# Performance work log

Hardware: AMD Instinct MI355X
Metric: run time of the kernel (lower is better)

The kernel has to match this reference:

```python
import jax, jax.numpy as jnp
import numpy as np

EPS = 1e-6
SCALING = 32 ** -0.5  # key_dim ** -0.5


def _ln(x, g, b):
    m = jnp.mean(x, -1, keepdims=True)
    v = jnp.var(x, -1, keepdims=True)
    return (x - m) * jax.lax.rsqrt(v + EPS) * g + b


def _dwconv(x, w, b, pad):
    # x: (B,H,W,C); w: (kh,kw,1,C) depthwise kernel
    y = jax.lax.conv_general_dilated(
        x, w, (1, 1), [(pad, pad), (pad, pad)],
        dimension_numbers=("NHWC", "HWIO", "NHWC"),
        feature_group_count=x.shape[-1])
    return y + b


def _rotate_every_two(x):
    x1 = x[..., ::2]
    x2 = x[..., 1::2]
    return jnp.stack([-x2, x1], axis=-1).reshape(x.shape)


def _theta_shift(x, sin, cos):
    return x * cos + _rotate_every_two(x) * sin


def setup_inputs() -> dict:
    key = jax.random.key(0)
    ks = jax.random.split(key, 32)
    B, H, W, C = 2, 56, 56, 256
    N, D = 8, C // 8          # heads, key_dim
    F = 1024                  # ffn_dim
    L = H * W
    g = 2 ** -2.5
    inp = {
        "x": jax.random.normal(ks[0], (B, H, W, C), jnp.float32),
        "sin": jax.random.normal(ks[1], (H, W, D), jnp.float32),
        "cos": jax.random.normal(ks[2], (H, W, D), jnp.float32),
        "mask": jax.random.normal(ks[3], (N, L, L), jnp.float32),
        # pos dwconv 3x3
        "pos_w": jax.random.normal(ks[4], (3, 3, 1, C), jnp.float32) * 0.05,
        "pos_b": jnp.zeros((C,), jnp.float32),
        # retention layernorm
        "ln1_g": jnp.ones((C,), jnp.float32),
        "ln1_b": jnp.zeros((C,), jnp.float32),
        # q/k/v projections (stored as (in,out))
        "wq": jax.random.normal(ks[5], (C, C), jnp.float32) * g * (2.0 / (C + C)) ** 0.5 * 10,
        "bq": jnp.zeros((C,), jnp.float32),
        "wk": jax.random.normal(ks[6], (C, C), jnp.float32) * g * 0.06,
        "bk": jnp.zeros((C,), jnp.float32),
        "wv": jax.random.normal(ks[7], (C, C), jnp.float32) * g * 0.06,
        "bv": jnp.zeros((C,), jnp.float32),
        # lepe dwconv 5x5
        "lepe_w": jax.random.normal(ks[8], (5, 5, 1, C), jnp.float32) * 0.05,
        "lepe_b": jnp.zeros((C,), jnp.float32),
        # out proj
        "wo": jax.random.normal(ks[9], (C, C), jnp.float32) * 0.06,
        "bo": jnp.zeros((C,), jnp.float32),
        # final layernorm
        "ln2_g": jnp.ones((C,), jnp.float32),
        "ln2_b": jnp.zeros((C,), jnp.float32),
        # ffn
        "w1": jax.random.normal(ks[10], (C, F), jnp.float32) * 0.04,
        "b1": jnp.zeros((F,), jnp.float32),
        "ffn_w": jax.random.normal(ks[11], (3, 3, 1, F), jnp.float32) * 0.05,
        "ffn_b": jnp.zeros((F,), jnp.float32),
        "w2": jax.random.normal(ks[12], (F, C), jnp.float32) * 0.04,
        "b2": jnp.zeros((C,), jnp.float32),
    }
    return inp


def _forward(x, sin, cos, mask, pos_w, pos_b, ln1_g, ln1_b, wq, bq, wk, bk,
             wv, bv, lepe_w, lepe_b, wo, bo, ln2_g, ln2_b, w1, b1,
             ffn_w, ffn_b, w2, b2):
    B, H, W, C = x.shape
    N = mask.shape[0]
    D = C // N
    L = H * W

    # positional dwconv residual
    x = x + _dwconv(x, pos_w, pos_b, 1)

    # ---- retention (VisionRetentionAll) ----
    y = _ln(x, ln1_g, ln1_b)
    q = y @ wq + bq
    k = (y @ wk + bk) * SCALING
    v = y @ wv + bv
    lepe = _dwconv(v, lepe_w, lepe_b, 2)

    # (B,H,W,C) -> (B,N,H,W,D)
    q = q.reshape(B, H, W, N, D).transpose(0, 3, 1, 2, 4)
    k = k.reshape(B, H, W, N, D).transpose(0, 3, 1, 2, 4)
    qr = _theta_shift(q, sin, cos).reshape(B, N, L, D)
    kr = _theta_shift(k, sin, cos).reshape(B, N, L, D)
    vr = v.reshape(B, H, W, N, D).transpose(0, 3, 1, 2, 4).reshape(B, N, L, D)

    qk = jnp.einsum("bnld,bnmd->bnlm", qr, kr) + mask  # (B,N,L,L)
    att = jax.nn.softmax(qk, axis=-1)
    out = jnp.einsum("bnlm,bnmd->bnld", att, vr)       # (B,N,L,D)
    out = out.transpose(0, 2, 1, 3).reshape(B, H, W, C)
    out = (out + lepe) @ wo + bo
    x = x + out

    # ---- FFN with depthwise conv ----
    z = _ln(x, ln2_g, ln2_b)
    z = jax.nn.gelu(z @ w1 + b1, approximate=False)
    z = z + _dwconv(z, ffn_w, ffn_b, 1)
    z = z @ w2 + b2
    return x + z


def reference(x, sin, cos, mask, pos_w, pos_b, ln1_g, ln1_b, wq, bq, wk, bk,
              wv, bv, lepe_w, lepe_b, wo, bo, ln2_g, ln2_b, w1, b1,
              ffn_w, ffn_b, w2, b2):
    return _forward(x, sin, cos, mask, pos_w, pos_b, ln1_g, ln1_b, wq, bq,
                    wk, bk, wv, bv, lepe_w, lepe_b, wo, bo, ln2_g, ln2_b,
                    w1, b1, ffn_w, ffn_b, w2, b2)
```

## Files before the change

kernel.cpp:

```cpp
#include <hip/hip_runtime.h>
#include <hip/hip_bf16.h>
#include <math.h>

#define Bn 2
#define Hn 56
#define Wn 56
#define Cn 256
#define Nh 8
#define Dh 32
#define Fn 1024
#define Ln (Hn*Wn)
#define Mrows (Bn*Ln)
#define SCALING_K 0.17677669529663687f

typedef __attribute__((ext_vector_type(4))) float f32x4;
typedef __attribute__((ext_vector_type(8))) short s16x8;
typedef unsigned short ushort_t;

__device__ __forceinline__ ushort_t f2bf(float f) {
    __hip_bfloat16 h = __float2bfloat16(f);
    return *reinterpret_cast<ushort_t*>(&h);
}

__global__ void dwconv_kernel(const float* __restrict__ in, const float* __restrict__ wgt,
                              const float* __restrict__ bias, float* __restrict__ out,
                              int C, int inld, int outld, int KS, int pad, int addin)
{
    int idx = blockIdx.x * blockDim.x + threadIdx.x;
    int c4 = C >> 2;
    int c = (idx % c4) << 2;
    int rest = idx / c4;
    int w = rest % Wn; rest /= Wn;
    int h = rest % Hn;
    int b = rest / Hn;
    if (b >= Bn) return;
    float4 acc = *(const float4*)&bias[c];
    for (int dh = 0; dh < KS; ++dh) {
        int hh = h + dh - pad;
        if (hh < 0 || hh >= Hn) continue;
        for (int dw = 0; dw < KS; ++dw) {
            int ww = w + dw - pad;
            if (ww < 0 || ww >= Wn) continue;
            float4 xv = *(const float4*)&in[(((size_t)b*Hn + hh)*Wn + ww)*inld + c];
            float4 wv = *(const float4*)&wgt[(size_t)(dh*KS + dw)*C + c];
            acc.x += xv.x*wv.x; acc.y += xv.y*wv.y; acc.z += xv.z*wv.z; acc.w += xv.w*wv.w;
        }
    }
    size_t oidx = (((size_t)b*Hn + h)*Wn + w);
    if (addin) {
        float4 xv = *(const float4*)&in[oidx*inld + c];
        acc.x += xv.x; acc.y += xv.y; acc.z += xv.z; acc.w += xv.w;
    }
    *(float4*)&out[oidx*outld + c] = acc;
}

__global__ __launch_bounds__(256) void ln_kernel(const float* __restrict__ in,
    const float* __restrict__ g, const float* __restrict__ b, float* __restrict__ out)
{
    int row = blockIdx.x;
    int t = threadIdx.x;
    float v = in[(size_t)row*Cn + t];
    float s1 = v, s2 = v*v;
    for (int m = 1; m < 64; m <<= 1) {
        s1 += __shfl_xor(s1, m);
        s2 += __shfl_xor(s2, m);
    }
    __shared__ float w1s[4], w2s[4];
    if ((t & 63) == 0) { w1s[t>>6] = s1; w2s[t>>6] = s2; }
    __syncthreads();
    s1 = w1s[0]+w1s[1]+w1s[2]+w1s[3];
    s2 = w2s[0]+w2s[1]+w2s[2]+w2s[3];
    float mean = s1 * (1.0f/Cn);
    float var  = s2 * (1.0f/Cn) - mean*mean;
    float r = rsqrtf(var + 1e-6f);
    out[(size_t)row*Cn + t] = (v - mean) * r * g[t] + b[t];
}

__global__ void prep_weights(const float* __restrict__ wq, const float* __restrict__ bq,
                             const float* __restrict__ wk, const float* __restrict__ bk,
                             const float* __restrict__ wv, const float* __restrict__ bv,
                             const float* __restrict__ wo, const float* __restrict__ w1,
                             const float* __restrict__ w2,
                             ushort_t* __restrict__ wqkvT, float* __restrict__ bqkv,
                             ushort_t* __restrict__ woT, ushort_t* __restrict__ w1T,
                             ushort_t* __restrict__ w2T)
{
    int idx = blockIdx.x * 256 + threadIdx.x;
    if (idx < 196608) {
        int j = idx >> 8, k = idx & 255;
        float v;
        if (j < 256)      v = wq[k*256 + j];
        else if (j < 512) v = wk[k*256 + (j-256)] * SCALING_K;
        else              v = wv[k*256 + (j-512)];
        wqkvT[idx] = f2bf(v);
    } else if (idx < 262144) {
        int r = idx - 196608;
        int j = r >> 8, k = r & 255;
        woT[r] = f2bf(wo[k*256 + j]);
    } else if (idx < 524288) {
        int r = idx - 262144;
        int j = r >> 8, k = r & 255;
        w1T[r] = f2bf(w1[k*1024 + j]);
    } else if (idx < 786432) {
        int r = idx - 524288;
        int j = r >> 10, k = r & 1023;
        w2T[r] = f2bf(w2[k*256 + j]);
    } else if (idx < 787200) {
        int j = idx - 786432;
        bqkv[j] = (j < 256) ? bq[j] : (j < 512 ? bk[j-256]*SCALING_K : bv[j-512]);
    }
}

__global__ __launch_bounds__(256) void gemm_bf16(
    const float* __restrict__ A, const float* __restrict__ A2, int lda,
    const ushort_t* __restrict__ BT, const float* __restrict__ bias,
    const float* __restrict__ resid, float* __restrict__ out, int ldo,
    int K, int gelu_flag)
{
    __shared__ __align__(16) ushort_t As[64][40];
    __shared__ __align__(16) ushort_t Bs[64][40];
    int t = threadIdx.x;
    int wid = t >> 6, lane = t & 63, l16 = lane & 15, quad = lane >> 4;
    int n0 = blockIdx.x << 6, m0 = blockIdx.y << 6;
    int srow = t >> 2, skc = (t & 3) << 3;
    f32x4 acc[4] = {{0,0,0,0},{0,0,0,0},{0,0,0,0},{0,0,0,0}};
    for (int k0 = 0; k0 < K; k0 += 32) {
        float av[8];
        const float* ap = &A[(size_t)(m0+srow)*lda + k0 + skc];
        *(float4*)&av[0] = *(const float4*)ap;
        *(float4*)&av[4] = *(const float4*)(ap + 4);
        if (A2) {
            const float* ap2 = &A2[(size_t)(m0+srow)*lda + k0 + skc];
            float4 x0 = *(const float4*)ap2;
            float4 x1 = *(const float4*)(ap2 + 4);
            av[0]+=x0.x; av[1]+=x0.y; av[2]+=x0.z; av[3]+=x0.w;
            av[4]+=x1.x; av[5]+=x1.y; av[6]+=x1.z; av[7]+=x1.w;
        }
        uint4 bv4 = *(const uint4*)&BT[(size_t)(n0+srow)*K + k0 + skc];
        ushort_t ac[8];
        #pragma unroll
        for (int i = 0; i < 8; ++i) ac[i] = f2bf(av[i]);
        __syncthreads();
        *(uint4*)&As[srow][skc] = *(uint4*)ac;
        *(uint4*)&Bs[srow][skc] = bv4;
        __syncthreads();
        s16x8 af = *(const s16x8*)&As[wid*16 + l16][quad*8];
        #pragma unroll
        for (int j = 0; j < 4; ++j) {
            s16x8 bf = *(const s16x8*)&Bs[j*16 + l16][quad*8];
            acc[j] = __builtin_amdgcn_mfma_f32_16x16x32_bf16(af, bf, acc[j], 0, 0, 0);
        }
    }
    #pragma unroll
    for (int j = 0; j < 4; ++j) {
        int col = n0 + j*16 + l16;
        float bv = bias[col];
        #pragma unroll
        for (int r = 0; r < 4; ++r) {
            int row = m0 + wid*16 + quad*4 + r;
            float v = acc[j][r] + bv;
            if (gelu_flag) v = 0.5f * v * (1.0f + erff(v * 0.70710678118654752f));
            size_t off = (size_t)row*ldo + col;
            if (resid) v += resid[off];
            out[off] = v;
        }
    }
}

__global__ __launch_bounds__(256) void pack_qkv(
    const float* __restrict__ qkv,
    const float* __restrict__ sp, const float* __restrict__ cp,
    ushort_t* __restrict__ qb, ushort_t* __restrict__ kb, ushort_t* __restrict__ vbT)
{
    __shared__ __align__(16) ushort_t Vl[64][40];
    int t = threadIdx.x;
    int l0 = blockIdx.x << 6;
    int n = blockIdx.y;
    int b = blockIdx.z;
    {
        int ll = t >> 2, dc = (t & 3) << 3;
        int l = l0 + ll;
        size_t gbase = ((size_t)(b*Ln + l))*768 + n*Dh + dc;
        float qx[8], kx[8], vx[8], sv[8], cv[8];
        *(float4*)&qx[0] = *(const float4*)&qkv[gbase];
        *(float4*)&qx[4] = *(const float4*)&qkv[gbase+4];
        *(float4*)&kx[0] = *(const float4*)&qkv[gbase+256];
        *(float4*)&kx[4] = *(const float4*)&qkv[gbase+260];
        *(float4*)&vx[0] = *(const float4*)&qkv[gbase+512];
        *(float4*)&vx[4] = *(const float4*)&qkv[gbase+516];
        size_t scb = (size_t)l*Dh + dc;
        *(float4*)&sv[0] = *(const float4*)&sp[scb];
        *(float4*)&sv[4] = *(const float4*)&sp[scb+4];
        *(float4*)&cv[0] = *(const float4*)&cp[scb];
        *(float4*)&cv[4] = *(const float4*)&cp[scb+4];
        ushort_t qo[8], ko[8], vo[8];
        #pragma unroll
        for (int j = 0; j < 8; j += 2) {
            float q0 = qx[j]*cv[j] - qx[j+1]*sv[j];
            float q1 = qx[j+1]*cv[j+1] + qx[j]*sv[j+1];
            float k0 = kx[j]*cv[j] - kx[j+1]*sv[j];
            float k1 = kx[j+1]*cv[j+1] + kx[j]*sv[j+1];
            qo[j] = f2bf(q0); qo[j+1] = f2bf(q1);
            ko[j] = f2bf(k0); ko[j+1] = f2bf(k1);
            vo[j] = f2bf(vx[j]); vo[j+1] = f2bf(vx[j+1]);
        }
        size_t hbase = ((size_t)((b*Nh + n)*Ln + l))*Dh + dc;
        *(uint4*)&qb[hbase] = *(uint4*)qo;
        *(uint4*)&kb[hbase] = *(uint4*)ko;
        *(uint4*)&Vl[ll][dc] = *(uint4*)vo;
    }
    __syncthreads();
    {
        int d = t >> 3, lc = (t & 7) << 3;
        ushort_t tmp[8];
        #pragma unroll
        for (int i = 0; i < 8; ++i) tmp[i] = Vl[lc + i][d];
        size_t tbase = ((size_t)((b*Nh + n)*Dh + d))*Ln + l0 + lc;
        *(uint4*)&vbT[tbase] = *(uint4*)tmp;
    }
}

__global__ __launch_bounds__(512) void flash_mfma(
    const ushort_t* __restrict__ qb, const ushort_t* __restrict__ kb,
    const ushort_t* __restrict__ vbT, const float* __restrict__ mask,
    float* __restrict__ out)
{
    __shared__ __align__(16) ushort_t Kt[2][64][40];
    __shared__ __align__(16) ushort_t Vt[2][32][72];
    __shared__ __align__(16) ushort_t Ps[8][16][72];
    int t = threadIdx.x;
    int wid = t >> 6, lane = t & 63, l16 = lane & 15, quad = lane >> 4;
    int bb = wid & 1, wq16 = wid >> 1;
    int l0 = blockIdx.x << 6;
    int n = blockIdx.y;

    const ushort_t* qbp = qb + ((size_t)(bb*Nh + n))*Ln*Dh;
    s16x8 qfrag = *(const s16x8*)(qbp + (size_t)(l0 + wq16*16 + l16)*Dh + quad*8);
    const float* mbase = mask + (size_t)n*Ln*Ln + (size_t)(l0 + wq16*16 + quad*4)*Ln;

    int sb   = t >> 8;
    int krow = (t >> 2) & 63, kkc = (t & 3) << 3;
    int vrow = (t >> 3) & 31, vkc = (t & 7) << 3;
    const ushort_t* kst = kb  + ((size_t)(sb*Nh + n))*Ln*Dh;
    const ushort_t* vst = vbT + ((size_t)((sb*Nh + n)*Dh + vrow))*Ln;

    f32x4 O0 = {0.f,0.f,0.f,0.f}, O1 = {0.f,0.f,0.f,0.f};
    float m_[4], l_[4];
    #pragma unroll
    for (int r = 0; r < 4; ++r) { m_[r] = -INFINITY; l_[r] = 0.f; }

    for (int m0 = 0; m0 < Ln; m0 += 64) {
        __syncthreads();
        *(uint4*)&Kt[sb][krow][kkc] = *(const uint4*)(kst + (size_t)(m0 + krow)*Dh + kkc);
        *(uint4*)&Vt[sb][vrow][vkc] = *(const uint4*)(vst + m0 + vkc);
        __syncthreads();

        f32x4 c0, c1, c2, c3;
        #pragma unroll
        for (int r = 0; r < 4; ++r) {
            const float* mr = mbase + (size_t)r*Ln + m0 + l16;
            c0[r] = mr[0]; c1[r] = mr[16]; c2[r] = mr[32]; c3[r] = mr[48];
        }
        f32x4 S[4];
        {
            s16x8 kf0 = *(const s16x8*)&Kt[bb][ 0 + l16][quad*8];
            s16x8 kf1 = *(const s16x8*)&Kt[bb][16 + l16][quad*8];
            s16x8 kf2 = *(const s16x8*)&Kt[bb][32 + l16][quad*8];
            s16x8 kf3 = *(const s16x8*)&Kt[bb][48 + l16][quad*8];
            S[0] = __builtin_amdgcn_mfma_f32_16x16x32_bf16(qfrag, kf0, c0, 0, 0, 0);
            S[1] = __builtin_amdgcn_mfma_f32_16x16x32_bf16(qfrag, kf1, c1, 0, 0, 0);
            S[2] = __builtin_amdgcn_mfma_f32_16x16x32_bf16(qfrag, kf2, c2, 0, 0, 0);
            S[3] = __builtin_amdgcn_mfma_f32_16x16x32_bf16(qfrag, kf3, c3, 0, 0, 0);
        }
        #pragma unroll
        for (int r = 0; r < 4; ++r) {
            float tm = fmaxf(fmaxf(S[0][r], S[1][r]), fmaxf(S[2][r], S[3][r]));
            tm = fmaxf(tm, __shfl_xor(tm, 1));
            tm = fmaxf(tm, __shfl_xor(tm, 2));
            tm = fmaxf(tm, __shfl_xor(tm, 4));
            tm = fmaxf(tm, __shfl_xor(tm, 8));
            float nm = fmaxf(m_[r], tm);
            float al = __expf(m_[r] - nm);
            m_[r] = nm;
            float p0 = __expf(S[0][r] - nm);
            float p1 = __expf(S[1][r] - nm);
            float p2 = __expf(S[2][r] - nm);
            float p3 = __expf(S[3][r] - nm);
            float ps = p0 + p1 + p2 + p3;
            ps += __shfl_xor(ps, 1); ps += __shfl_xor(ps, 2);
            ps += __shfl_xor(ps, 4); ps += __shfl_xor(ps, 8);
            l_[r] = l_[r]*al + ps;
            O0[r] *= al; O1[r] *= al;
            int rr = quad*4 + r;
            Ps[wid][rr][ 0 + l16] = f2bf(p0);
            Ps[wid][rr][16 + l16] = f2bf(p1);
            Ps[wid][rr][32 + l16] = f2bf(p2);
            Ps[wid][rr][48 + l16] = f2bf(p3);
        }
        #pragma unroll
        for (int kc = 0; kc < 2; ++kc) {
            s16x8 pf  = *(const s16x8*)&Ps[wid][l16][kc*32 + quad*8];
            s16x8 vf0 = *(const s16x8*)&Vt[bb][ 0 + l16][kc*32 + quad*8];
            s16x8 vf1 = *(const s16x8*)&Vt[bb][16 + l16][kc*32 + quad*8];
            O0 = __builtin_amdgcn_mfma_f32_16x16x32_bf16(pf, vf0, O0, 0, 0, 0);
            O1 = __builtin_amdgcn_mfma_f32_16x16x32_bf16(pf, vf1, O1, 0, 0, 0);
        }
    }
    #pragma unroll
    for (int r = 0; r < 4; ++r) {
        float inv = 1.0f / l_[r];
        size_t row = (size_t)(bb*Ln + l0 + wq16*16 + quad*4 + r)*Cn + n*Dh;
        out[row + l16]      = O0[r] * inv;
        out[row + 16 + l16] = O1[r] * inv;
    }
}

extern "C" void kernel_launch(void* const* d_in, const int* in_sizes, int n_in,
                              void* d_out, int out_size, void* d_ws, size_t ws_size,
                              hipStream_t stream) {
    const float* x     = (const float*)d_in[0];
    const float* sinp  = (const float*)d_in[1];
    const float* cosp  = (const float*)d_in[2];
    const float* mask  = (const float*)d_in[3];
    const float* pos_w = (const float*)d_in[4];
    const float* pos_b = (const float*)d_in[5];
    const float* ln1_g = (const float*)d_in[6];
    const float* ln1_b = (const float*)d_in[7];
    const float* wq = (const float*)d_in[8];
    const float* bq = (const float*)d_in[9];
    const float* wk = (const float*)d_in[10];
    const float* bk = (const float*)d_in[11];
    const float* wv = (const float*)d_in[12];
    const float* bv = (const float*)d_in[13];
    const float* lepe_w = (const float*)d_in[14];
    const float* lepe_b = (const float*)d_in[15];
    const float* wo = (const float*)d_in[16];
    const float* bo = (const float*)d_in[17];
    const float* ln2_g = (const float*)d_in[18];
    const float* ln2_b = (const float*)d_in[19];
    const float* w1 = (const float*)d_in[20];
    const float* b1 = (const float*)d_in[21];
    const float* ffn_w = (const float*)d_in[22];
    const float* ffn_b = (const float*)d_in[23];
    const float* w2 = (const float*)d_in[24];
    const float* b2 = (const float*)d_in[25];

    float* ws = (float*)d_ws;
    const size_t MC = (size_t)Mrows*Cn;
    float* xbuf = ws;
    float* qkv  = ws + MC;
    float* ybuf = ws + 4*MC;
    float* lepe = ws + 5*MC;
    float* x2   = ws + 6*MC;
    float* att  = ws + 7*MC;
    float* z1   = ws + 8*MC;
    float* z2   = ws + 12*MC;
    ushort_t* qb  = (ushort_t*)(ws + 16*MC);
    ushort_t* kb  = (ushort_t*)(ws + 16*MC + MC/2);
    ushort_t* vbT = (ushort_t*)(ws + 17*MC);
    float* wtb = ws + 17*MC + MC/2;
    ushort_t* wqkvT = (ushort_t*)wtb;
    ushort_t* woT   = (ushort_t*)(wtb + 98304);
    ushort_t* w1T   = (ushort_t*)(wtb + 131072);
    ushort_t* w2T   = (ushort_t*)(wtb + 262144);
    float*    bqkv  = wtb + 393216;
    float* outp = (float*)d_out;

    int totalC = Mrows*Cn/4;
    int totalF = Mrows*Fn/4;
    dim3 fg(Ln/64, Nh, Bn);
    dim3 fg2(Ln/64, Nh);

    prep_weights<<<(787200+255)/256, 256, 0, stream>>>(wq,bq,wk,bk,wv,bv,wo,w1,w2,
                                                       wqkvT,bqkv,woT,w1T,w2T);
    dwconv_kernel<<<(totalC+255)/256, 256, 0, stream>>>(x, pos_w, pos_b, xbuf, Cn, Cn, Cn, 3, 1, 1);
    ln_kernel<<<Mrows, 256, 0, stream>>>(xbuf, ln1_g, ln1_b, ybuf);
    gemm_bf16<<<dim3(12, Mrows/64), 256, 0, stream>>>(ybuf, nullptr, Cn, wqkvT, bqkv,
                                                      nullptr, qkv, 768, Cn, 0);
    pack_qkv<<<fg, 256, 0, stream>>>(qkv, sinp, cosp, qb, kb, vbT);
    dwconv_kernel<<<(totalC+255)/256, 256, 0, stream>>>(qkv+512, lepe_w, lepe_b, lepe, Cn, 768, Cn, 5, 2, 0);
    flash_mfma<<<fg2, 512, 0, stream>>>(qb, kb, vbT, mask, att);
    gemm_bf16<<<dim3(4, Mrows/64), 256, 0, stream>>>(att, lepe, Cn, woT, bo, xbuf, x2, Cn, Cn, 0);
    ln_kernel<<<Mrows, 256, 0, stream>>>(x2, ln2_g, ln2_b, ybuf);
    gemm_bf16<<<dim3(16, Mrows/64), 256, 0, stream>>>(ybuf, nullptr, Cn, w1T, b1, nullptr, z1, Fn, Cn, 1);
    dwconv_kernel<<<(totalF+255)/256, 256, 0, stream>>>(z1, ffn_w, ffn_b, z2, Fn, Fn, Fn, 3, 1, 1);
    gemm_bf16<<<dim3(4, Mrows/64), 256, 0, stream>>>(z2, nullptr, Fn, w2T, b2, x2, outp, Cn, Fn, 0);
}
```

Baseline: 683.5 us.

## Fuse layernorm into GEMMs, register-block dwconvs, prefetch flash tiles, tile weight transpose

Replaces the weight prep with a shared-memory tiled transpose kernel. Folds layernorm into the GEMM A-load using precomputed per-row mean and rstd, and fuses the first stats pass into the positional dwconv. Rewrites the depthwise convs to compute four output pixels per thread with reused input registers, and makes the FFN dwconv write bf16 so the last GEMM reads half the bytes. The flash attention loop now prefetches the next K/V tile and mask values into registers. This removes the normalized intermediate buffers and redundant loads, at the cost of more registers and LN arithmetic repeated across GEMM column blocks.

```diff
diff --git a/kernel.cpp b/kernel.cpp
--- a/kernel.cpp
+++ b/kernel.cpp
@@ -22,45 +22,187 @@
     return *reinterpret_cast<ushort_t*>(&h);
 }
 
-__global__ void dwconv_kernel(const float* __restrict__ in, const float* __restrict__ wgt,
-                              const float* __restrict__ bias, float* __restrict__ out,
-                              int C, int inld, int outld, int KS, int pad, int addin)
-{
-    int idx = blockIdx.x * blockDim.x + threadIdx.x;
-    int c4 = C >> 2;
-    int c = (idx % c4) << 2;
-    int rest = idx / c4;
-    int w = rest % Wn; rest /= Wn;
-    int h = rest % Hn;
-    int b = rest / Hn;
-    if (b >= Bn) return;
-    float4 acc = *(const float4*)&bias[c];
+__global__ __launch_bounds__(256) void transpose_w(
+    const float* __restrict__ wq, const float* __restrict__ wk, const float* __restrict__ wv,
+    const float* __restrict__ wo, const float* __restrict__ w1, const float* __restrict__ w2,
+    ushort_t* __restrict__ wqkvT, ushort_t* __restrict__ woT,
+    ushort_t* __restrict__ w1T, ushort_t* __restrict__ w2T)
+{
+    int z = blockIdx.z;
+    const float* src; ushort_t* dst; int K, N; float scale = 1.f;
+    switch (z) {
+      case 0: src=wq; dst=wqkvT;           K=256;  N=256;  break;
+      case 1: src=wk; dst=wqkvT+256*256;   K=256;  N=256;  scale=SCALING_K; break;
+      case 2: src=wv; dst=wqkvT+512*256;   K=256;  N=256;  break;
+      case 3: src=wo; dst=woT;             K=256;  N=256;  break;
+      case 4: src=w1; dst=w1T;             K=256;  N=1024; break;
+      default: src=w2; dst=w2T;            K=1024; N=256;  break;
+    }
+    int n0 = blockIdx.x << 5, k0 = blockIdx.y << 5;
+    if (n0 >= N || k0 >= K) return;
+    __shared__ float tile[32][33];
+    int tx = threadIdx.x & 31, ty = threadIdx.x >> 5;
+    #pragma unroll
+    for (int r = 0; r < 4; ++r)
+        tile[ty + 8*r][tx] = src[(size_t)(k0 + ty + 8*r)*N + n0 + tx] * scale;
+    __syncthreads();
+    #pragma unroll
+    for (int r = 0; r < 4; ++r)
+        dst[(size_t)(n0 + ty + 8*r)*K + k0 + tx] = f2bf(tile[tx][ty + 8*r]);
+}
+
+__global__ void prep_bias(const float* __restrict__ bq, const float* __restrict__ bk,
+                          const float* __restrict__ bv, float* __restrict__ bqkv)
+{
+    int i = blockIdx.x*256 + threadIdx.x;
+    if (i < 768)
+        bqkv[i] = (i < 256) ? bq[i] : (i < 512 ? bk[i-256]*SCALING_K : bv[i-512]);
+}
+
+__global__ __launch_bounds__(256) void dwconv_ln(
+    const float* __restrict__ x, const float* __restrict__ wgt, const float* __restrict__ bias,
+    float* __restrict__ out, float2* __restrict__ stats)
+{
+    int t = threadIdx.x;
+    int cg = t & 63;
+    int g = blockIdx.x*4 + (t >> 6);
+    int w0 = (g % 14) << 2;
+    int hr = g / 14;
+    int h = hr % Hn;
+    int c = cg << 2;
+    float4 wv9[9];
+    #pragma unroll
+    for (int i = 0; i < 9; ++i) wv9[i] = *(const float4*)&wgt[i*Cn + c];
+    float4 bias4 = *(const float4*)&bias[c];
+    float4 acc[4] = {bias4, bias4, bias4, bias4};
+    const float* base = x + (size_t)(hr - h)*Wn*Cn + c;
+    #pragma unroll
+    for (int dh = 0; dh < 3; ++dh) {
+        int hh = h + dh - 1;
+        if (hh < 0 || hh >= Hn) continue;
+        const float* rowp = base + (size_t)hh*Wn*Cn;
+        float4 xv[6];
+        #pragma unroll
+        for (int j = 0; j < 6; ++j) {
+            int wc = w0 - 1 + j;
+            xv[j] = (wc >= 0 && wc < Wn) ? *(const float4*)&rowp[(size_t)wc*Cn]
+                                         : make_float4(0.f,0.f,0.f,0.f);
+        }
+        #pragma unroll
+        for (int dw = 0; dw < 3; ++dw) {
+            float4 wv = wv9[dh*3 + dw];
+            #pragma unroll
+            for (int p = 0; p < 4; ++p) {
+                acc[p].x += xv[p+dw].x*wv.x; acc[p].y += xv[p+dw].y*wv.y;
+                acc[p].z += xv[p+dw].z*wv.z; acc[p].w += xv[p+dw].w*wv.w;
+            }
+        }
+        if (dh == 1) {
+            #pragma unroll
+            for (int p = 0; p < 4; ++p) {
+                acc[p].x += xv[p+1].x; acc[p].y += xv[p+1].y;
+                acc[p].z += xv[p+1].z; acc[p].w += xv[p+1].w;
+            }
+        }
+    }
+    float s[4], q[4];
+    #pragma unroll
+    for (int p = 0; p < 4; ++p) {
+        s[p] = acc[p].x + acc[p].y + acc[p].z + acc[p].w;
+        q[p] = acc[p].x*acc[p].x + acc[p].y*acc[p].y + acc[p].z*acc[p].z + acc[p].w*acc[p].w;
+    }
+    #pragma unroll
+    for (int m = 1; m < 64; m <<= 1) {
+        #pragma unroll
+        for (int p = 0; p < 4; ++p) {
+            s[p] += __shfl_xor(s[p], m);
+            q[p] += __shfl_xor(q[p], m);
+        }
+    }
+    size_t pixbase = (size_t)hr*Wn + w0;
+    #pragma unroll
+    for (int p = 0; p < 4; ++p)
+        *(float4*)&out[(pixbase + p)*Cn + c] = acc[p];
+    if (cg == 0) {
+        #pragma unroll
+        for (int p = 0; p < 4; ++p) {
+            float mean = s[p] * (1.0f/Cn);
+            float var  = q[p] * (1.0f/Cn) - mean*mean;
+            stats[pixbase + p] = make_float2(mean, rsqrtf(var + 1e-6f));
+        }
+    }
+}
+
+template<int KS, int OBF>
+__global__ __launch_bounds__(256) void dwconv4(
+    const float* __restrict__ in, const float* __restrict__ wgt, const float* __restrict__ bias,
+    void* __restrict__ outv, int C, int inld, int addin)
+{
+    constexpr int PAD = KS/2;
+    int t = threadIdx.x;
+    int cgs = C >> 2;
+    int qpb = 256 / cgs;
+    int cg = t % cgs;
+    int g = blockIdx.x*qpb + t/cgs;
+    int w0 = (g % 14) << 2;
+    int hr = g / 14;
+    int h = hr % Hn;
+    int c = cg << 2;
+    float4 bias4 = *(const float4*)&bias[c];
+    float4 acc[4] = {bias4, bias4, bias4, bias4};
+    const float* base = in + (size_t)(hr - h)*Wn*inld + c;
+    #pragma unroll
     for (int dh = 0; dh < KS; ++dh) {
-        int hh = h + dh - pad;
+        int hh = h + dh - PAD;
         if (hh < 0 || hh >= Hn) continue;
+        const float* rowp = base + (size_t)hh*Wn*inld;
+        float4 xv[KS+3];
+        #pragma unroll
+        for (int j = 0; j < KS+3; ++j) {
+            int wc = w0 - PAD + j;
+            xv[j] = (wc >= 0 && wc < Wn) ? *(const float4*)&rowp[(size_t)wc*inld]
+                                         : make_float4(0.f,0.f,0.f,0.f);
+        }
+        #pragma unroll
         for (int dw = 0; dw < KS; ++dw) {
-            int ww = w + dw - pad;
-            if (ww < 0 || ww >= Wn) continue;
-            float4 xv = *(const float4*)&in[(((size_t)b*Hn + hh)*Wn + ww)*inld + c];
-            float4 wv = *(const float4*)&wgt[(size_t)(dh*KS + dw)*C + c];
-            acc.x += xv.x*wv.x; acc.y += xv.y*wv.y; acc.z += xv.z*wv.z; acc.w += xv.w*wv.w;
-        }
-    }
-    size_t oidx = (((size_t)b*Hn + h)*Wn + w);
-    if (addin) {
-        float4 xv = *(const float4*)&in[oidx*inld + c];
-        acc.x += xv.x; acc.y += xv.y; acc.z += xv.z; acc.w += xv.w;
-    }
-    *(float4*)&out[oidx*outld + c] = acc;
-}
-
-__global__ __launch_bounds__(256) void ln_kernel(const float* __restrict__ in,
-    const float* __restrict__ g, const float* __restrict__ b, float* __restrict__ out)
+            float4 wv = *(const float4*)&wgt[(dh*KS + dw)*C + c];
+            #pragma unroll
+            for (int p = 0; p < 4; ++p) {
+                acc[p].x += xv[p+dw].x*wv.x; acc[p].y += xv[p+dw].y*wv.y;
+                acc[p].z += xv[p+dw].z*wv.z; acc[p].w += xv[p+dw].w*wv.w;
+            }
+        }
+        if (addin && dh == PAD) {
+            #pragma unroll
+            for (int p = 0; p < 4; ++p) {
+                acc[p].x += xv[p+PAD].x; acc[p].y += xv[p+PAD].y;
+                acc[p].z += xv[p+PAD].z; acc[p].w += xv[p+PAD].w;
+            }
+        }
+    }
+    size_t pixbase = (size_t)hr*Wn + w0;
+    if (OBF) {
+        ushort_t* outb = (ushort_t*)outv;
+        #pragma unroll
+        for (int p = 0; p < 4; ++p) {
+            ushort_t tmp[4] = { f2bf(acc[p].x), f2bf(acc[p].y), f2bf(acc[p].z), f2bf(acc[p].w) };
+            *(uint2*)&outb[(pixbase + p)*C + c] = *(uint2*)tmp;
+        }
+    } else {
+        float* outf = (float*)outv;
+        #pragma unroll
+        for (int p = 0; p < 4; ++p)
+            *(float4*)&outf[(pixbase + p)*C + c] = acc[p];
+    }
+}
+
+__global__ __launch_bounds__(256) void ln_stats(const float* __restrict__ in, float2* __restrict__ stats)
 {
     int row = blockIdx.x;
     int t = threadIdx.x;
     float v = in[(size_t)row*Cn + t];
     float s1 = v, s2 = v*v;
+    #pragma unroll
     for (int m = 1; m < 64; m <<= 1) {
         s1 += __shfl_xor(s1, m);
         s2 += __shfl_xor(s2, m);
@@ -68,51 +210,18 @@
     __shared__ float w1s[4], w2s[4];
     if ((t & 63) == 0) { w1s[t>>6] = s1; w2s[t>>6] = s2; }
     __syncthreads();
-    s1 = w1s[0]+w1s[1]+w1s[2]+w1s[3];
-    s2 = w2s[0]+w2s[1]+w2s[2]+w2s[3];
-    float mean = s1 * (1.0f/Cn);
-    float var  = s2 * (1.0f/Cn) - mean*mean;
-    float r = rsqrtf(var + 1e-6f);
-    out[(size_t)row*Cn + t] = (v - mean) * r * g[t] + b[t];
-}
-
-__global__ void prep_weights(const float* __restrict__ wq, const float* __restrict__ bq,
-                             const float* __restrict__ wk, const float* __restrict__ bk,
-                             const float* __restrict__ wv, const float* __restrict__ bv,
-                             const float* __restrict__ wo, const float* __restrict__ w1,
-                             const float* __restrict__ w2,
-                             ushort_t* __restrict__ wqkvT, float* __restrict__ bqkv,
-                             ushort_t* __restrict__ woT, ushort_t* __restrict__ w1T,
-                             ushort_t* __restrict__ w2T)
-{
-    int idx = blockIdx.x * 256 + threadIdx.x;
-    if (idx < 196608) {
-        int j = idx >> 8, k = idx & 255;
-        float v;
-        if (j < 256)      v = wq[k*256 + j];
-        else if (j < 512) v = wk[k*256 + (j-256)] * SCALING_K;
-        else              v = wv[k*256 + (j-512)];
-        wqkvT[idx] = f2bf(v);
-    } else if (idx < 262144) {
-        int r = idx - 196608;
-        int j = r >> 8, k = r & 255;
-        woT[r] = f2bf(wo[k*256 + j]);
-    } else if (idx < 524288) {
-        int r = idx - 262144;
-        int j = r >> 8, k = r & 255;
-        w1T[r] = f2bf(w1[k*1024 + j]);
-    } else if (idx < 786432) {
-        int r = idx - 524288;
-        int j = r >> 10, k = r & 1023;
-        w2T[r] = f2bf(w2[k*256 + j]);
-    } else if (idx < 787200) {
-        int j = idx - 786432;
-        bqkv[j] = (j < 256) ? bq[j] : (j < 512 ? bk[j-256]*SCALING_K : bv[j-512]);
+    if (t == 0) {
+        s1 = w1s[0]+w1s[1]+w1s[2]+w1s[3];
+        s2 = w2s[0]+w2s[1]+w2s[2]+w2s[3];
+        float mean = s1 * (1.0f/Cn);
+        float var  = s2 * (1.0f/Cn) - mean*mean;
+        stats[row] = make_float2(mean, rsqrtf(var + 1e-6f));
     }
 }
 
 __global__ __launch_bounds__(256) void gemm_bf16(
-    const float* __restrict__ A, const float* __restrict__ A2, int lda,
+    const void* __restrict__ Av, int abf16, const float* __restrict__ A2, int lda,
+    const float2* __restrict__ lnstat, const float* __restrict__ lng, const float* __restrict__ lnb,
     const ushort_t* __restrict__ BT, const float* __restrict__ bias,
     const float* __restrict__ resid, float* __restrict__ out, int ldo,
     int K, int gelu_flag)
@@ -123,23 +232,39 @@
     int wid = t >> 6, lane = t & 63, l16 = lane & 15, quad = lane >> 4;
     int n0 = blockIdx.x << 6, m0 = blockIdx.y << 6;
     int srow = t >> 2, skc = (t & 3) << 3;
+    float2 st = make_float2(0.f, 1.f);
+    if (lnstat) st = lnstat[m0 + srow];
     f32x4 acc[4] = {{0,0,0,0},{0,0,0,0},{0,0,0,0},{0,0,0,0}};
     for (int k0 = 0; k0 < K; k0 += 32) {
-        float av[8];
-        const float* ap = &A[(size_t)(m0+srow)*lda + k0 + skc];
-        *(float4*)&av[0] = *(const float4*)ap;
-        *(float4*)&av[4] = *(const float4*)(ap + 4);
-        if (A2) {
-            const float* ap2 = &A2[(size_t)(m0+srow)*lda + k0 + skc];
-            float4 x0 = *(const float4*)ap2;
-            float4 x1 = *(const float4*)(ap2 + 4);
-            av[0]+=x0.x; av[1]+=x0.y; av[2]+=x0.z; av[3]+=x0.w;
-            av[4]+=x1.x; av[5]+=x1.y; av[6]+=x1.z; av[7]+=x1.w;
+        ushort_t ac[8];
+        if (abf16) {
+            *(uint4*)ac = *(const uint4*)&((const ushort_t*)Av)[(size_t)(m0+srow)*lda + k0 + skc];
+        } else {
+            float av[8];
+            const float* ap = &((const float*)Av)[(size_t)(m0+srow)*lda + k0 + skc];
+            *(float4*)&av[0] = *(const float4*)ap;
+            *(float4*)&av[4] = *(const float4*)(ap + 4);
+            if (A2) {
+                const float* ap2 = &A2[(size_t)(m0+srow)*lda + k0 + skc];
+                float4 x0 = *(const float4*)ap2;
+                float4 x1 = *(const float4*)(ap2 + 4);
+                av[0]+=x0.x; av[1]+=x0.y; av[2]+=x0.z; av[3]+=x0.w;
+                av[4]+=x1.x; av[5]+=x1.y; av[6]+=x1.z; av[7]+=x1.w;
+            }
+            if (lnstat) {
+                float gg[8], bb[8];
+                *(float4*)&gg[0] = *(const float4*)&lng[k0 + skc];
+                *(float4*)&gg[4] = *(const float4*)&lng[k0 + skc + 4];
+                *(float4*)&bb[0] = *(const float4*)&lnb[k0 + skc];
+                *(float4*)&bb[4] = *(const float4*)&lnb[k0 + skc + 4];
+                #pragma unroll
+                for (int i = 0; i < 8; ++i)
+                    av[i] = (av[i] - st.x)*st.y*gg[i] + bb[i];
+            }
+            #pragma unroll
+            for (int i = 0; i < 8; ++i) ac[i] = f2bf(av[i]);
         }
         uint4 bv4 = *(const uint4*)&BT[(size_t)(n0+srow)*K + k0 + skc];
-        ushort_t ac[8];
-        #pragma unroll
-        for (int i = 0; i < 8; ++i) ac[i] = f2bf(av[i]);
         __syncthreads();
         *(uint4*)&As[srow][skc] = *(uint4*)ac;
         *(uint4*)&Bs[srow][skc] = bv4;
@@ -249,18 +374,34 @@
     #pragma unroll
     for (int r = 0; r < 4; ++r) { m_[r] = -INFINITY; l_[r] = 0.f; }
 
+    uint4 kreg = *(const uint4*)(kst + (size_t)krow*Dh + kkc);
+    uint4 vreg = *(const uint4*)(vst + vkc);
+    f32x4 c0, c1, c2, c3;
+    #pragma unroll
+    for (int r = 0; r < 4; ++r) {
+        const float* mr = mbase + (size_t)r*Ln + l16;
+        c0[r] = mr[0]; c1[r] = mr[16]; c2[r] = mr[32]; c3[r] = mr[48];
+    }
+
     for (int m0 = 0; m0 < Ln; m0 += 64) {
         __syncthreads();
-        *(uint4*)&Kt[sb][krow][kkc] = *(const uint4*)(kst + (size_t)(m0 + krow)*Dh + kkc);
-        *(uint4*)&Vt[sb][vrow][vkc] = *(const uint4*)(vst + m0 + vkc);
+        *(uint4*)&Kt[sb][krow][kkc] = kreg;
+        *(uint4*)&Vt[sb][vrow][vkc] = vreg;
         __syncthreads();
 
-        f32x4 c0, c1, c2, c3;
-        #pragma unroll
-        for (int r = 0; r < 4; ++r) {
-            const float* mr = mbase + (size_t)r*Ln + m0 + l16;
-            c0[r] = mr[0]; c1[r] = mr[16]; c2[r] = mr[32]; c3[r] = mr[48];
-        }
+        int m1 = m0 + 64;
+        uint4 krn = kreg, vrn = vreg;
+        f32x4 d0 = c0, d1 = c1, d2 = c2, d3 = c3;
+        if (m1 < Ln) {
+            krn = *(const uint4*)(kst + (size_t)(m1 + krow)*Dh + kkc);
+            vrn = *(const uint4*)(vst + m1 + vkc);
+            #pragma unroll
+            for (int r = 0; r < 4; ++r) {
+                const float* mr = mbase + (size_t)r*Ln + m1 + l16;
+                d0[r] = mr[0]; d1[r] = mr[16]; d2[r] = mr[32]; d3[r] = mr[48];
+            }
+        }
+
         f32x4 S[4];
         {
             s16x8 kf0 = *(const s16x8*)&Kt[bb][ 0 + l16][quad*8];
@@ -305,6 +446,8 @@
             O0 = __builtin_amdgcn_mfma_f32_16x16x32_bf16(pf, vf0, O0, 0, 0, 0);
             O1 = __builtin_amdgcn_mfma_f32_16x16x32_bf16(pf, vf1, O1, 0, 0, 0);
         }
+        kreg = krn; vreg = vrn;
+        c0 = d0; c1 = d1; c2 = d2; c3 = d3;
     }
     #pragma unroll
     for (int r = 0; r < 4; ++r) {
@@ -349,40 +492,38 @@
     const size_t MC = (size_t)Mrows*Cn;
     float* xbuf = ws;
     float* qkv  = ws + MC;
-    float* ybuf = ws + 4*MC;
-    float* lepe = ws + 5*MC;
-    float* x2   = ws + 6*MC;
-    float* att  = ws + 7*MC;
-    float* z1   = ws + 8*MC;
-    float* z2   = ws + 12*MC;
-    ushort_t* qb  = (ushort_t*)(ws + 16*MC);
-    ushort_t* kb  = (ushort_t*)(ws + 16*MC + MC/2);
-    ushort_t* vbT = (ushort_t*)(ws + 17*MC);
-    float* wtb = ws + 17*MC + MC/2;
+    float* lepe = ws + 4*MC;
+    float* x2   = ws + 5*MC;
+    float* att  = ws + 6*MC;
+    float* z1   = ws + 7*MC;
+    ushort_t* z2bf = (ushort_t*)(ws + 11*MC);
+    ushort_t* qb   = (ushort_t*)(ws + 13*MC);
+    ushort_t* kb   = (ushort_t*)(ws + 13*MC + MC/2);
+    ushort_t* vbT  = (ushort_t*)(ws + 14*MC);
+    float* wtb = ws + 14*MC + MC/2;
     ushort_t* wqkvT = (ushort_t*)wtb;
     ushort_t* woT   = (ushort_t*)(wtb + 98304);
     ushort_t* w1T   = (ushort_t*)(wtb + 131072);
     ushort_t* w2T   = (ushort_t*)(wtb + 262144);
     float*    bqkv  = wtb + 393216;
+    float2*   stats1 = (float2*)(wtb + 394240);
+    float2*   stats2 = (float2*)(wtb + 406784);
     float* outp = (float*)d_out;
 
-    int totalC = Mrows*Cn/4;
-    int totalF = Mrows*Fn/4;
-    dim3 fg(Ln/64, Nh, Bn);
-    dim3 fg2(Ln/64, Nh);
-
-    prep_weights<<<(787200+255)/256, 256, 0, stream>>>(wq,bq,wk,bk,wv,bv,wo,w1,w2,
-                                                       wqkvT,bqkv,woT,w1T,w2T);
-    dwconv_kernel<<<(totalC+255)/256, 256, 0, stream>>>(x, pos_w, pos_b, xbuf, Cn, Cn, Cn, 3, 1, 1);
-    ln_kernel<<<Mrows, 256, 0, stream>>>(xbuf, ln1_g, ln1_b, ybuf);
-    gemm_bf16<<<dim3(12, Mrows/64), 256, 0, stream>>>(ybuf, nullptr, Cn, wqkvT, bqkv,
-                                                      nullptr, qkv, 768, Cn, 0);
-    pack_qkv<<<fg, 256, 0, stream>>>(qkv, sinp, cosp, qb, kb, vbT);
-    dwconv_kernel<<<(totalC+255)/256, 256, 0, stream>>>(qkv+512, lepe_w, lepe_b, lepe, Cn, 768, Cn, 5, 2, 0);
-    flash_mfma<<<fg2, 512, 0, stream>>>(qb, kb, vbT, mask, att);
-    gemm_bf16<<<dim3(4, Mrows/64), 256, 0, stream>>>(att, lepe, Cn, woT, bo, xbuf, x2, Cn, Cn, 0);
-    ln_kernel<<<Mrows, 256, 0, stream>>>(x2, ln2_g, ln2_b, ybuf);
-    gemm_bf16<<<dim3(16, Mrows/64), 256, 0, stream>>>(ybuf, nullptr, Cn, w1T, b1, nullptr, z1, Fn, Cn, 1);
-    dwconv_kernel<<<(totalF+255)/256, 256, 0, stream>>>(z1, ffn_w, ffn_b, z2, Fn, Fn, Fn, 3, 1, 1);
-    gemm_bf16<<<dim3(4, Mrows/64), 256, 0, stream>>>(z2, nullptr, Fn, w2T, b2, x2, outp, Cn, Fn, 0);
-}
+    transpose_w<<<dim3(32,32,6), 256, 0, stream>>>(wq,wk,wv,wo,w1,w2, wqkvT,woT,w1T,w2T);
+    prep_bias<<<3, 256, 0, stream>>>(bq,bk,bv,bqkv);
+    dwconv_ln<<<Mrows/16, 256, 0, stream>>>(x, pos_w, pos_b, xbuf, stats1);
+    gemm_bf16<<<dim3(12, Mrows/64), 256, 0, stream>>>(xbuf, 0, nullptr, Cn,
+        stats1, ln1_g, ln1_b, wqkvT, bqkv, nullptr, qkv, 768, Cn, 0);
+    pack_qkv<<<dim3(Ln/64, Nh, Bn), 256, 0, stream>>>(qkv, sinp, cosp, qb, kb, vbT);
+    dwconv4<5,0><<<Mrows/16, 256, 0, stream>>>(qkv+512, lepe_w, lepe_b, lepe, Cn, 768, 0);
+    flash_mfma<<<dim3(Ln/64, Nh), 512, 0, stream>>>(qb, kb, vbT, mask, att);
+    gemm_bf16<<<dim3(4, Mrows/64), 256, 0, stream>>>(att, 0, lepe, Cn,
+        nullptr, nullptr, nullptr, woT, bo, xbuf, x2, Cn, Cn, 0);
+    ln_stats<<<Mrows, 256, 0, stream>>>(x2, stats2);
+    gemm_bf16<<<dim3(16, Mrows/64), 256, 0, stream>>>(x2, 0, nullptr, Cn,
+        stats2, ln2_g, ln2_b, w1T, b1, nullptr, z1, Fn, Cn, 1);
+    dwconv4<3,1><<<Mrows/4, 256, 0, stream>>>(z1, ffn_w, ffn_b, z2bf, Fn, Fn, 1);
+    gemm_bf16<<<dim3(4, Mrows/64), 256, 0, stream>>>(z2bf, 1, nullptr, Fn,
+        nullptr, nullptr, nullptr, w2T, b2, x2, outp, Cn, Fn, 0);
+}
```

Result: faster. 657.8 us (-3.8%).
